# Kernel optimization log

Hardware: AMD Instinct MI355X
Metric: run time of the kernel (lower is better)

The kernel has to match this reference:

```python
import jax, jax.numpy as jnp
import numpy as np

B, N_ATOMS, D_ATOM = 64, 256, 256
T_ANGLES = 2048
D_HID, D_OUT = 512, 256
BN_EPS = 1e-5


def setup_inputs() -> dict:
    key = jax.random.key(0)
    ks = jax.random.split(key, 8)
    z = jax.random.normal(ks[0], (B, N_ATOMS, D_ATOM), dtype=jnp.float32)
    # all entries valid (>=0) so the nonzero-selected row set is all B*T rows
    angel_atom_table = jax.random.randint(ks[1], (B, T_ANGLES, 3), 0, N_ATOMS, dtype=jnp.int64)
    W1 = jax.random.normal(ks[2], (D_ATOM, D_HID), dtype=jnp.float32) * (1.0 / np.sqrt(D_ATOM))
    b1 = jax.random.normal(ks[3], (D_HID,), dtype=jnp.float32) * 0.01
    gamma = jnp.ones((D_HID,), dtype=jnp.float32)
    beta = jnp.zeros((D_HID,), dtype=jnp.float32)
    W2 = jax.random.normal(ks[4], (D_HID, D_OUT), dtype=jnp.float32) * (1.0 / np.sqrt(D_HID))
    b2 = jax.random.normal(ks[5], (D_OUT,), dtype=jnp.float32) * 0.01
    return {"z": z, "angel_atom_table": angel_atom_table, "W1": W1, "b1": b1,
            "gamma": gamma, "beta": beta, "W2": W2, "b2": b2}


def reference(z, angel_atom_table, W1, b1, gamma, beta, W2, b2):
    Bb, Tt, _ = angel_atom_table.shape
    bi = jnp.arange(Bb)[:, None]                       # [B,1] broadcast batch index
    # gather 3 atom embeddings per angle and sum -> [B,T,d_atom]
    x = (z[bi, angel_atom_table[:, :, 0]]
         + z[bi, angel_atom_table[:, :, 1]]
         + z[bi, angel_atom_table[:, :, 2]])
    x = x.reshape(Bb * Tt, -1)                         # flattened valid rows (all valid)
    h = x @ W1 + b1                                    # Linear(d_atom, d_hid)
    mean = jnp.mean(h, axis=0)                         # BatchNorm1d (batch stats)
    var = jnp.var(h, axis=0)
    h = (h - mean) * jax.lax.rsqrt(var + BN_EPS) * gamma + beta
    h = jax.nn.relu(h)                                 # dropout inactive (eval)
    out = h @ W2 + b2                                  # Linear(d_hid, d_output)
    return out
```

## Files before the change

### kernel.cpp

```cpp
#include <hip/hip_runtime.h>

static constexpr int Bn  = 64;
static constexpr int T   = 2048;
static constexpr int NA  = 256;
static constexpr int DA  = 256;
static constexpr int DH  = 512;
static constexpr int DO  = 256;
static constexpr int M   = Bn * T;
static constexpr int NBS = M / 128;
static constexpr int NBC = M / 64;

typedef __attribute__((ext_vector_type(4))) float  f32x4;
typedef __attribute__((ext_vector_type(8))) __bf16 bf16x8;
typedef __attribute__((ext_vector_type(8))) short  short8;

__device__ __forceinline__ unsigned short f2bf(float f) {
  union { float f; unsigned u; } v; v.f = f;
  unsigned u = v.u + 0x7FFFu + ((v.u >> 16) & 1u);
  return (unsigned short)(u >> 16);
}
__device__ __forceinline__ float bf2f(unsigned short b) {
  union { unsigned u; float f; } v; v.u = ((unsigned)b) << 16;
  return v.f;
}

__device__ __forceinline__ void gl_lds16(const void* g, void* l) {
  __builtin_amdgcn_global_load_lds(
      (const __attribute__((address_space(1))) unsigned int*)g,
      (__attribute__((address_space(3))) unsigned int*)l, 16, 0, 0);
}

__global__ void prep_kernel(const float* __restrict__ W1, const float* __restrict__ W2,
                            unsigned short* __restrict__ W1T, unsigned short* __restrict__ W2T) {
  int id = blockIdx.x * 256 + threadIdx.x;
  {
    int n = id >> 8, k = id & 255;
    W1T[id] = f2bf(W1[k * DH + n]);
  }
  {
    int n = id >> 9, k = id & 511;
    W2T[id] = f2bf(W2[k * DO + n]);
  }
}

__global__ __launch_bounds__(256) void kA_zw(
    const float* __restrict__ z, const unsigned short* __restrict__ W1T,
    unsigned short* __restrict__ zW) {
  __shared__ __align__(16) unsigned short As[32][64][8];
  __shared__ __align__(16) unsigned short Bs[2][4][256][8];
  const int tid = threadIdx.x;
  const int bm = blockIdx.x >> 1, bn = blockIdx.x & 1;
  const int row0 = bm * 64, n0b = bn * 256;
  const int wave = tid >> 6, lane = tid & 63, ql = lane >> 4, r16 = lane & 15;
  const int gr = tid >> 2, sub = tid & 3;
  const int sxw = (sub << 2) ^ sub;
  const int sxr = (ql << 2) ^ ql;

  auto stageB = [&](int buf, int k0) {
#pragma unroll
    for (int i = 0; i < 4; ++i)
      gl_lds16(W1T + (size_t)(n0b + tid) * DA + k0 + i * 8,
               (unsigned short*)Bs + (size_t)((buf * 4 + i) * 256 + wave * 64) * 8);
  };

  stageB(0, 0);

  {
    const float* zr = z + (size_t)(row0 + gr) * DA + sub * 8;
    f32x4 za[16];
#pragma unroll
    for (int c = 0; c < 8; ++c) {
      za[2 * c]     = *(const f32x4*)(zr + c * 32);
      za[2 * c + 1] = *(const f32x4*)(zr + c * 32 + 4);
    }
#pragma unroll
    for (int c = 0; c < 8; ++c) {
      bf16x8 pk;
#pragma unroll
      for (int j = 0; j < 4; ++j) {
        pk[j]     = (__bf16)za[2 * c][j];
        pk[4 + j] = (__bf16)za[2 * c + 1][j];
      }
      *(bf16x8*)&As[c * 4 + sub][gr ^ sxw][0] = pk;
    }
  }
  asm volatile("s_waitcnt lgkmcnt(0)" ::: "memory");
  __builtin_amdgcn_s_barrier();

  f32x4 acc[4][4] = {};
  for (int s = 0; s < 8; ++s) {
    asm volatile("s_waitcnt lgkmcnt(0)" ::: "memory");
    if (s < 7) {
      stageB((s + 1) & 1, (s + 1) * 32);
      asm volatile("s_waitcnt vmcnt(4)" ::: "memory");
    } else {
      asm volatile("s_waitcnt vmcnt(0)" ::: "memory");
    }
    bf16x8 afr[4], bfr[4];
#pragma unroll
    for (int mf = 0; mf < 4; ++mf)
      afr[mf] = *(const bf16x8*)&As[s * 4 + ql][(mf * 16 + r16) ^ sxr][0];
#pragma unroll
    for (int nf = 0; nf < 4; ++nf)
      bfr[nf] = *(const bf16x8*)&Bs[s & 1][ql][wave * 64 + nf * 16 + r16][0];
    __builtin_amdgcn_s_setprio(1);
#pragma unroll
    for (int mf = 0; mf < 4; ++mf)
#pragma unroll
      for (int nf = 0; nf < 4; ++nf)
        acc[mf][nf] = __builtin_amdgcn_mfma_f32_16x16x32_bf16(afr[mf], bfr[nf], acc[mf][nf], 0, 0, 0);
    __builtin_amdgcn_s_setprio(0);
  }

  const int n0 = n0b + wave * 64;
#pragma unroll
  for (int nf = 0; nf < 4; ++nf) {
    const int col = n0 + nf * 16 + r16;
#pragma unroll
    for (int mf = 0; mf < 4; ++mf)
#pragma unroll
      for (int p = 0; p < 4; ++p)
        zW[(size_t)(row0 + mf * 16 + ql * 4 + p) * DH + col] = f2bf(acc[mf][nf][p]);
  }
}

__global__ __launch_bounds__(256) void kB_stats(
    const unsigned short* __restrict__ zW, const int* __restrict__ tbl,
    float* __restrict__ psum, float* __restrict__ psq) {
  __shared__ int idxs[128][3];
  __shared__ float red1[4][512];
  __shared__ float red2[4][512];
  const int bid = blockIdx.x;
  const int blk = (bid & 7) * (NBS >> 3) + (bid >> 3);
  const int tid = threadIdx.x;
  const int row0 = blk * 128;
  const unsigned short* zWb = zW + (size_t)(row0 >> 11) * NA * DH;

  for (int i = tid; i < 384; i += 256) ((int*)idxs)[i] = tbl[(size_t)row0 * 3 + i];
  __syncthreads();

  const int cc = tid & 63, rg = tid >> 6;
  float s1[8] = {0, 0, 0, 0, 0, 0, 0, 0};
  float s2[8] = {0, 0, 0, 0, 0, 0, 0, 0};
#pragma unroll 8
  for (int i = 0; i < 32; ++i) {
    const int r = rg * 32 + i;
    const unsigned short* p0 = zWb + (size_t)idxs[r][0] * DH + cc * 8;
    const unsigned short* p1 = zWb + (size_t)idxs[r][1] * DH + cc * 8;
    const unsigned short* p2 = zWb + (size_t)idxs[r][2] * DH + cc * 8;
    short8 v0 = *(const short8*)p0;
    short8 v1 = *(const short8*)p1;
    short8 v2 = *(const short8*)p2;
#pragma unroll
    for (int j = 0; j < 8; ++j) {
      float h = bf2f((unsigned short)v0[j]) + bf2f((unsigned short)v1[j]) + bf2f((unsigned short)v2[j]);
      s1[j] += h;
      s2[j] = fmaf(h, h, s2[j]);
    }
  }
#pragma unroll
  for (int j = 0; j < 8; ++j) { red1[rg][cc * 8 + j] = s1[j]; red2[rg][cc * 8 + j] = s2[j]; }
  __syncthreads();
  for (int c = tid; c < 512; c += 256) {
    psum[(size_t)c * NBS + blk] = red1[0][c] + red1[1][c] + red1[2][c] + red1[3][c];
    psq [(size_t)c * NBS + blk] = red2[0][c] + red2[1][c] + red2[2][c] + red2[3][c];
  }
}

__global__ void k2_stats(const float* __restrict__ psum, const float* __restrict__ psq,
                         const float* __restrict__ gamma, const float* __restrict__ beta,
                         float* __restrict__ coef) {
  const int col = blockIdx.x, lane = threadIdx.x;
  float s1 = 0.f, s2 = 0.f;
  for (int i = lane; i < NBS; i += 64) {
    s1 += psum[(size_t)col * NBS + i];
    s2 += psq [(size_t)col * NBS + i];
  }
#pragma unroll
  for (int d = 1; d < 64; d <<= 1) { s1 += __shfl_xor(s1, d); s2 += __shfl_xor(s2, d); }
  if (lane == 0) {
    const float inv = 1.0f / (float)M;
    float mean = s1 * inv;
    float var  = s2 * inv - mean * mean;
    float a = gamma[col] * rsqrtf(var + 1e-5f);
    coef[col]      = a;
    coef[DH + col] = beta[col] - mean * a;
  }
}

__global__ __launch_bounds__(256) void kC_out(
    const unsigned short* __restrict__ zW, const int* __restrict__ tbl,
    const unsigned short* __restrict__ W2T, const float* __restrict__ coef,
    const float* __restrict__ b2, float* __restrict__ out) {
  __shared__ __align__(16) unsigned short As[32][64][8];
  __shared__ __align__(16) unsigned short Bs[2][4][256][8];
  __shared__ float aC[DH], dC[DH], bC[DO];
  __shared__ int idxs[64][3];

  const int bid = blockIdx.x;
  const int blk = (bid & 7) * (NBC >> 3) + (bid >> 3);
  const int tid = threadIdx.x;
  const int row0 = blk * 64;
  const unsigned short* zWb = zW + (size_t)(row0 >> 11) * NA * DH;

  if (tid < 192) ((int*)idxs)[tid] = tbl[(size_t)row0 * 3 + tid];
  aC[tid]       = coef[tid];            aC[tid + 256] = coef[tid + 256];
  dC[tid]       = coef[DH + tid];       dC[tid + 256] = coef[DH + tid + 256];
  bC[tid]       = b2[tid];
  __syncthreads();

  const int wave = tid >> 6, lane = tid & 63, ql = lane >> 4, r16 = lane & 15;
  const int gr = tid >> 2, sub = tid & 3;
  const int sxw = (sub << 2) ^ sub;
  const int sxr = (ql << 2) ^ ql;

  const unsigned short* g0p = zWb + (size_t)idxs[gr][0] * DH + sub * 8;
  const unsigned short* g1p = zWb + (size_t)idxs[gr][1] * DH + sub * 8;
  const unsigned short* g2p = zWb + (size_t)idxs[gr][2] * DH + sub * 8;

  auto stageB = [&](int buf, int k0) {
#pragma unroll
    for (int i = 0; i < 4; ++i)
      gl_lds16(W2T + (size_t)tid * DH + k0 + i * 8,
               (unsigned short*)Bs + (size_t)((buf * 4 + i) * 256 + wave * 64) * 8);
  };

  stageB(0, 0);

  f32x4 acc[4][4] = {};

  for (int h = 0; h < 2; ++h) {
    const int kh = h * 256;
    short8 v0[8], v1[8], v2[8];
#pragma unroll
    for (int c = 0; c < 8; ++c) {
      v0[c] = *(const short8*)(g0p + kh + c * 32);
      v1[c] = *(const short8*)(g1p + kh + c * 32);
      v2[c] = *(const short8*)(g2p + kh + c * 32);
    }
    if (h) {
      asm volatile("s_waitcnt lgkmcnt(0)" ::: "memory");
      __builtin_amdgcn_s_barrier();
    }
#pragma unroll
    for (int c = 0; c < 8; ++c) {
      const int kk = kh + c * 32 + sub * 8;
      f32x4 av0 = *(const f32x4*)&aC[kk];
      f32x4 av1 = *(const f32x4*)&aC[kk + 4];
      f32x4 dv0 = *(const f32x4*)&dC[kk];
      f32x4 dv1 = *(const f32x4*)&dC[kk + 4];
      bf16x8 pk;
#pragma unroll
      for (int j = 0; j < 4; ++j) {
        float h0 = bf2f((unsigned short)v0[c][j]) + bf2f((unsigned short)v1[c][j]) + bf2f((unsigned short)v2[c][j]);
        float f0 = fmaf(h0, av0[j], dv0[j]);
        f0 = f0 > 0.f ? f0 : 0.f;
        pk[j] = (__bf16)f0;
        float h1 = bf2f((unsigned short)v0[c][4 + j]) + bf2f((unsigned short)v1[c][4 + j]) + bf2f((unsigned short)v2[c][4 + j]);
        float f1 = fmaf(h1, av1[j], dv1[j]);
        f1 = f1 > 0.f ? f1 : 0.f;
        pk[4 + j] = (__bf16)f1;
      }
      *(bf16x8*)&As[c * 4 + sub][gr ^ sxw][0] = pk;
    }
    asm volatile("s_waitcnt lgkmcnt(0)" ::: "memory");
    __builtin_amdgcn_s_barrier();

    for (int s = 0; s < 8; ++s) {
      const int sg = h * 8 + s;
      asm volatile("s_waitcnt lgkmcnt(0)" ::: "memory");
      if (sg < 15) {
        stageB((sg + 1) & 1, (sg + 1) * 32);
        asm volatile("s_waitcnt vmcnt(4)" ::: "memory");
      } else {
        asm volatile("s_waitcnt vmcnt(0)" ::: "memory");
      }
      bf16x8 afr[4], bfr[4];
#pragma unroll
      for (int mf = 0; mf < 4; ++mf)
        afr[mf] = *(const bf16x8*)&As[s * 4 + ql][(mf * 16 + r16) ^ sxr][0];
#pragma unroll
      for (int nf = 0; nf < 4; ++nf)
        bfr[nf] = *(const bf16x8*)&Bs[sg & 1][ql][wave * 64 + nf * 16 + r16][0];
      __builtin_amdgcn_s_setprio(1);
#pragma unroll
      for (int mf = 0; mf < 4; ++mf)
#pragma unroll
        for (int nf = 0; nf < 4; ++nf)
          acc[mf][nf] = __builtin_amdgcn_mfma_f32_16x16x32_bf16(afr[mf], bfr[nf], acc[mf][nf], 0, 0, 0);
      __builtin_amdgcn_s_setprio(0);
    }
  }

  const int n0 = wave * 64;
#pragma unroll
  for (int nf = 0; nf < 4; ++nf) {
    const int col = n0 + nf * 16 + r16;
    const float bv = bC[col];
#pragma unroll
    for (int mf = 0; mf < 4; ++mf)
#pragma unroll
      for (int p = 0; p < 4; ++p)
        out[(size_t)(row0 + mf * 16 + ql * 4 + p) * DO + col] = acc[mf][nf][p] + bv;
  }
}

extern "C" void kernel_launch(void* const* d_in, const int* in_sizes, int n_in,
                              void* d_out, int out_size, void* d_ws, size_t ws_size,
                              hipStream_t stream) {
  const float* z     = (const float*)d_in[0];
  const int*   tbl   = (const int*)d_in[1];
  const float* W1    = (const float*)d_in[2];
  const float* gamma = (const float*)d_in[4];
  const float* beta  = (const float*)d_in[5];
  const float* W2    = (const float*)d_in[6];
  const float* b2    = (const float*)d_in[7];
  float* out = (float*)d_out;

  char* ws = (char*)d_ws;
  unsigned short* W1T  = (unsigned short*)(ws);
  unsigned short* W2T  = (unsigned short*)(ws + (256 << 10));
  float*          coef = (float*)(ws + (512 << 10));
  float*          psum = (float*)(ws + (1 << 20));
  float*          psq  = (float*)(ws + (3 << 20));
  unsigned short* zW   = (unsigned short*)(ws + (16 << 20));

  prep_kernel<<<512, 256, 0, stream>>>(W1, W2, W1T, W2T);
  kA_zw<<<512, 256, 0, stream>>>(z, W1T, zW);
  kB_stats<<<NBS, 256, 0, stream>>>(zW, tbl, psum, psq);
  k2_stats<<<DH, 64, 0, stream>>>(psum, psq, gamma, beta, coef);
  kC_out<<<NBC, 256, 0, stream>>>(zW, tbl, W2T, coef, b2, out);
}
```

Before: 272.1 us.

## Load GEMM B operands directly into registers and drop LDS staging of weights

Both GEMM kernels now read the bf16 weight fragments straight from global memory into registers with a two-step register double buffer, replacing the global-to-LDS async staging. This shrinks LDS use, and kC gets a launch bound of 3 blocks per SM to raise occupancy. kA remaps block indices so each XCD works on a contiguous range of row blocks. kB_stats uses 64-row blocks, doubling the grid and the partial-sum buffers. The risks are extra register pressure and repeated uncached-in-LDS weight reads per wave, which now rely on L2.

New measurement: 268.8 us. About the same (-1.2%).

```diff
diff --git a/kernel.cpp b/kernel.cpp
--- a/kernel.cpp
+++ b/kernel.cpp
@@ -7,7 +7,7 @@
 static constexpr int DH  = 512;
 static constexpr int DO  = 256;
 static constexpr int M   = Bn * T;
-static constexpr int NBS = M / 128;
+static constexpr int NBS = M / 64;
 static constexpr int NBC = M / 64;
 
 typedef __attribute__((ext_vector_type(4))) float  f32x4;
@@ -22,12 +22,6 @@
 __device__ __forceinline__ float bf2f(unsigned short b) {
   union { unsigned u; float f; } v; v.u = ((unsigned)b) << 16;
   return v.f;
-}
-
-__device__ __forceinline__ void gl_lds16(const void* g, void* l) {
-  __builtin_amdgcn_global_load_lds(
-      (const __attribute__((address_space(1))) unsigned int*)g,
-      (__attribute__((address_space(3))) unsigned int*)l, 16, 0, 0);
 }
 
 __global__ void prep_kernel(const float* __restrict__ W1, const float* __restrict__ W2,
@@ -47,62 +41,47 @@
     const float* __restrict__ z, const unsigned short* __restrict__ W1T,
     unsigned short* __restrict__ zW) {
   __shared__ __align__(16) unsigned short As[32][64][8];
-  __shared__ __align__(16) unsigned short Bs[2][4][256][8];
   const int tid = threadIdx.x;
-  const int bm = blockIdx.x >> 1, bn = blockIdx.x & 1;
+  const int xcd = blockIdx.x & 7, idx = blockIdx.x >> 3;
+  const int bm = xcd * 32 + (idx >> 1), bn = idx & 1;
   const int row0 = bm * 64, n0b = bn * 256;
   const int wave = tid >> 6, lane = tid & 63, ql = lane >> 4, r16 = lane & 15;
   const int gr = tid >> 2, sub = tid & 3;
   const int sxw = (sub << 2) ^ sub;
   const int sxr = (ql << 2) ^ ql;
 
-  auto stageB = [&](int buf, int k0) {
-#pragma unroll
-    for (int i = 0; i < 4; ++i)
-      gl_lds16(W1T + (size_t)(n0b + tid) * DA + k0 + i * 8,
-               (unsigned short*)Bs + (size_t)((buf * 4 + i) * 256 + wave * 64) * 8);
-  };
-
-  stageB(0, 0);
+  const unsigned short* bp = W1T + (size_t)(n0b + wave * 64 + r16) * DA + ql * 8;
+
+  bf16x8 bq[2][4];
+#pragma unroll
+  for (int p = 0; p < 2; ++p)
+#pragma unroll
+    for (int nf = 0; nf < 4; ++nf)
+      bq[p][nf] = *(const bf16x8*)(bp + nf * 16 * DA + p * 32);
 
   {
     const float* zr = z + (size_t)(row0 + gr) * DA + sub * 8;
-    f32x4 za[16];
 #pragma unroll
     for (int c = 0; c < 8; ++c) {
-      za[2 * c]     = *(const f32x4*)(zr + c * 32);
-      za[2 * c + 1] = *(const f32x4*)(zr + c * 32 + 4);
-    }
-#pragma unroll
-    for (int c = 0; c < 8; ++c) {
+      f32x4 a0 = *(const f32x4*)(zr + c * 32);
+      f32x4 a1 = *(const f32x4*)(zr + c * 32 + 4);
       bf16x8 pk;
 #pragma unroll
-      for (int j = 0; j < 4; ++j) {
-        pk[j]     = (__bf16)za[2 * c][j];
-        pk[4 + j] = (__bf16)za[2 * c + 1][j];
-      }
+      for (int j = 0; j < 4; ++j) { pk[j] = (__bf16)a0[j]; pk[4 + j] = (__bf16)a1[j]; }
       *(bf16x8*)&As[c * 4 + sub][gr ^ sxw][0] = pk;
     }
   }
-  asm volatile("s_waitcnt lgkmcnt(0)" ::: "memory");
-  __builtin_amdgcn_s_barrier();
+  __syncthreads();
 
   f32x4 acc[4][4] = {};
+#pragma unroll
   for (int s = 0; s < 8; ++s) {
-    asm volatile("s_waitcnt lgkmcnt(0)" ::: "memory");
-    if (s < 7) {
-      stageB((s + 1) & 1, (s + 1) * 32);
-      asm volatile("s_waitcnt vmcnt(4)" ::: "memory");
-    } else {
-      asm volatile("s_waitcnt vmcnt(0)" ::: "memory");
-    }
     bf16x8 afr[4], bfr[4];
 #pragma unroll
     for (int mf = 0; mf < 4; ++mf)
       afr[mf] = *(const bf16x8*)&As[s * 4 + ql][(mf * 16 + r16) ^ sxr][0];
 #pragma unroll
-    for (int nf = 0; nf < 4; ++nf)
-      bfr[nf] = *(const bf16x8*)&Bs[s & 1][ql][wave * 64 + nf * 16 + r16][0];
+    for (int nf = 0; nf < 4; ++nf) bfr[nf] = bq[s & 1][nf];
     __builtin_amdgcn_s_setprio(1);
 #pragma unroll
     for (int mf = 0; mf < 4; ++mf)
@@ -110,6 +89,11 @@
       for (int nf = 0; nf < 4; ++nf)
         acc[mf][nf] = __builtin_amdgcn_mfma_f32_16x16x32_bf16(afr[mf], bfr[nf], acc[mf][nf], 0, 0, 0);
     __builtin_amdgcn_s_setprio(0);
+    if (s + 2 < 8) {
+#pragma unroll
+      for (int nf = 0; nf < 4; ++nf)
+        bq[s & 1][nf] = *(const bf16x8*)(bp + nf * 16 * DA + (s + 2) * 32);
+    }
   }
 
   const int n0 = n0b + wave * 64;
@@ -127,24 +111,24 @@
 __global__ __launch_bounds__(256) void kB_stats(
     const unsigned short* __restrict__ zW, const int* __restrict__ tbl,
     float* __restrict__ psum, float* __restrict__ psq) {
-  __shared__ int idxs[128][3];
+  __shared__ int idxs[64][3];
   __shared__ float red1[4][512];
   __shared__ float red2[4][512];
   const int bid = blockIdx.x;
   const int blk = (bid & 7) * (NBS >> 3) + (bid >> 3);
   const int tid = threadIdx.x;
-  const int row0 = blk * 128;
+  const int row0 = blk * 64;
   const unsigned short* zWb = zW + (size_t)(row0 >> 11) * NA * DH;
 
-  for (int i = tid; i < 384; i += 256) ((int*)idxs)[i] = tbl[(size_t)row0 * 3 + i];
+  if (tid < 192) ((int*)idxs)[tid] = tbl[(size_t)row0 * 3 + tid];
   __syncthreads();
 
   const int cc = tid & 63, rg = tid >> 6;
   float s1[8] = {0, 0, 0, 0, 0, 0, 0, 0};
   float s2[8] = {0, 0, 0, 0, 0, 0, 0, 0};
 #pragma unroll 8
-  for (int i = 0; i < 32; ++i) {
-    const int r = rg * 32 + i;
+  for (int i = 0; i < 16; ++i) {
+    const int r = rg * 16 + i;
     const unsigned short* p0 = zWb + (size_t)idxs[r][0] * DH + cc * 8;
     const unsigned short* p1 = zWb + (size_t)idxs[r][1] * DH + cc * 8;
     const unsigned short* p2 = zWb + (size_t)idxs[r][2] * DH + cc * 8;
@@ -188,13 +172,12 @@
   }
 }
 
-__global__ __launch_bounds__(256) void kC_out(
+__global__ __launch_bounds__(256, 3) void kC_out(
     const unsigned short* __restrict__ zW, const int* __restrict__ tbl,
     const unsigned short* __restrict__ W2T, const float* __restrict__ coef,
     const float* __restrict__ b2, float* __restrict__ out) {
   __shared__ __align__(16) unsigned short As[32][64][8];
-  __shared__ __align__(16) unsigned short Bs[2][4][256][8];
-  __shared__ float aC[DH], dC[DH], bC[DO];
+  __shared__ float aC[DH], dC[DH];
   __shared__ int idxs[64][3];
 
   const int bid = blockIdx.x;
@@ -206,7 +189,6 @@
   if (tid < 192) ((int*)idxs)[tid] = tbl[(size_t)row0 * 3 + tid];
   aC[tid]       = coef[tid];            aC[tid + 256] = coef[tid + 256];
   dC[tid]       = coef[DH + tid];       dC[tid + 256] = coef[DH + tid + 256];
-  bC[tid]       = b2[tid];
   __syncthreads();
 
   const int wave = tid >> 6, lane = tid & 63, ql = lane >> 4, r16 = lane & 15;
@@ -218,32 +200,26 @@
   const unsigned short* g1p = zWb + (size_t)idxs[gr][1] * DH + sub * 8;
   const unsigned short* g2p = zWb + (size_t)idxs[gr][2] * DH + sub * 8;
 
-  auto stageB = [&](int buf, int k0) {
-#pragma unroll
-    for (int i = 0; i < 4; ++i)
-      gl_lds16(W2T + (size_t)tid * DH + k0 + i * 8,
-               (unsigned short*)Bs + (size_t)((buf * 4 + i) * 256 + wave * 64) * 8);
-  };
-
-  stageB(0, 0);
+  const unsigned short* bp = W2T + (size_t)(wave * 64 + r16) * DH + ql * 8;
+
+  bf16x8 bq[2][4];
+#pragma unroll
+  for (int p = 0; p < 2; ++p)
+#pragma unroll
+    for (int nf = 0; nf < 4; ++nf)
+      bq[p][nf] = *(const bf16x8*)(bp + nf * 16 * DH + p * 32);
 
   f32x4 acc[4][4] = {};
 
+#pragma unroll
   for (int h = 0; h < 2; ++h) {
     const int kh = h * 256;
-    short8 v0[8], v1[8], v2[8];
+    if (h) __builtin_amdgcn_s_barrier();
 #pragma unroll
     for (int c = 0; c < 8; ++c) {
-      v0[c] = *(const short8*)(g0p + kh + c * 32);
-      v1[c] = *(const short8*)(g1p + kh + c * 32);
-      v2[c] = *(const short8*)(g2p + kh + c * 32);
-    }
-    if (h) {
-      asm volatile("s_waitcnt lgkmcnt(0)" ::: "memory");
-      __builtin_amdgcn_s_barrier();
-    }
-#pragma unroll
-    for (int c = 0; c < 8; ++c) {
+      short8 v0 = *(const short8*)(g0p + kh + c * 32);
+      short8 v1 = *(const short8*)(g1p + kh + c * 32);
+      short8 v2 = *(const short8*)(g2p + kh + c * 32);
       const int kk = kh + c * 32 + sub * 8;
       f32x4 av0 = *(const f32x4*)&aC[kk];
       f32x4 av1 = *(const f32x4*)&aC[kk + 4];
@@ -252,11 +228,11 @@
       bf16x8 pk;
 #pragma unroll
       for (int j = 0; j < 4; ++j) {
-        float h0 = bf2f((unsigned short)v0[c][j]) + bf2f((unsigned short)v1[c][j]) + bf2f((unsigned short)v2[c][j]);
+        float h0 = bf2f((unsigned short)v0[j]) + bf2f((unsigned short)v1[j]) + bf2f((unsigned short)v2[j]);
         float f0 = fmaf(h0, av0[j], dv0[j]);
         f0 = f0 > 0.f ? f0 : 0.f;
         pk[j] = (__bf16)f0;
-        float h1 = bf2f((unsigned short)v0[c][4 + j]) + bf2f((unsigned short)v1[c][4 + j]) + bf2f((unsigned short)v2[c][4 + j]);
+        float h1 = bf2f((unsigned short)v0[4 + j]) + bf2f((unsigned short)v1[4 + j]) + bf2f((unsigned short)v2[4 + j]);
         float f1 = fmaf(h1, av1[j], dv1[j]);
         f1 = f1 > 0.f ? f1 : 0.f;
         pk[4 + j] = (__bf16)f1;
@@ -265,23 +241,17 @@
     }
     asm volatile("s_waitcnt lgkmcnt(0)" ::: "memory");
     __builtin_amdgcn_s_barrier();
-
+    __builtin_amdgcn_sched_barrier(0);
+
+#pragma unroll
     for (int s = 0; s < 8; ++s) {
       const int sg = h * 8 + s;
-      asm volatile("s_waitcnt lgkmcnt(0)" ::: "memory");
-      if (sg < 15) {
-        stageB((sg + 1) & 1, (sg + 1) * 32);
-        asm volatile("s_waitcnt vmcnt(4)" ::: "memory");
-      } else {
-        asm volatile("s_waitcnt vmcnt(0)" ::: "memory");
-      }
       bf16x8 afr[4], bfr[4];
 #pragma unroll
       for (int mf = 0; mf < 4; ++mf)
         afr[mf] = *(const bf16x8*)&As[s * 4 + ql][(mf * 16 + r16) ^ sxr][0];
 #pragma unroll
-      for (int nf = 0; nf < 4; ++nf)
-        bfr[nf] = *(const bf16x8*)&Bs[sg & 1][ql][wave * 64 + nf * 16 + r16][0];
+      for (int nf = 0; nf < 4; ++nf) bfr[nf] = bq[sg & 1][nf];
       __builtin_amdgcn_s_setprio(1);
 #pragma unroll
       for (int mf = 0; mf < 4; ++mf)
@@ -289,6 +259,11 @@
         for (int nf = 0; nf < 4; ++nf)
           acc[mf][nf] = __builtin_amdgcn_mfma_f32_16x16x32_bf16(afr[mf], bfr[nf], acc[mf][nf], 0, 0, 0);
       __builtin_amdgcn_s_setprio(0);
+      if (sg + 2 < 16) {
+#pragma unroll
+        for (int nf = 0; nf < 4; ++nf)
+          bq[sg & 1][nf] = *(const bf16x8*)(bp + nf * 16 * DH + (sg + 2) * 32);
+      }
     }
   }
 
@@ -296,7 +271,7 @@
 #pragma unroll
   for (int nf = 0; nf < 4; ++nf) {
     const int col = n0 + nf * 16 + r16;
-    const float bv = bC[col];
+    const float bv = b2[col];
 #pragma unroll
     for (int mf = 0; mf < 4; ++mf)
 #pragma unroll
@@ -321,8 +296,8 @@
   unsigned short* W1T  = (unsigned short*)(ws);
   unsigned short* W2T  = (unsigned short*)(ws + (256 << 10));
   float*          coef = (float*)(ws + (512 << 10));
-  float*          psum = (float*)(ws + (1 << 20));
-  float*          psq  = (float*)(ws + (3 << 20));
+  float*          psum = (float*)(ws + (2 << 20));
+  float*          psq  = (float*)(ws + (6 << 20));
   unsigned short* zW   = (unsigned short*)(ws + (16 << 20));
 
   prep_kernel<<<512, 256, 0, stream>>>(W1, W2, W1T, W2T);
```
